# Performance work log

Hardware: AMD Instinct MI355X
Metric: run time of the kernel (lower is better)

## Reference

```python
import jax, jax.numpy as jnp
import numpy as np

N, E, D = 50000, 500000, 128


def layer_norm(x, w, b, eps=1e-5):
    mu = jnp.mean(x, axis=-1, keepdims=True)
    var = jnp.var(x, axis=-1, keepdims=True)
    return (x - mu) * jax.lax.rsqrt(var + eps) * w + b


def setup_inputs() -> dict:
    key = jax.random.key(0)
    ks = jax.random.split(key, 8)
    z = jax.random.normal(ks[0], (N, D), dtype=jnp.float32)
    pot_arcs = jax.random.randint(ks[1], (E, 2), 0, N, dtype=jnp.int64)
    s = 1.0 / np.sqrt(D)
    lin1_w = jax.random.uniform(ks[2], (D, D), jnp.float32, -s, s)
    lin1_b = jax.random.uniform(ks[3], (D,), jnp.float32, -s, s)
    lin2_w = jax.random.uniform(ks[4], (D, D), jnp.float32, -s, s)
    lin2_b = jax.random.uniform(ks[5], (D,), jnp.float32, -s, s)
    bil_w = jax.random.uniform(ks[6], (1, D, D), jnp.float32, -s, s)
    bil_b = jax.random.uniform(ks[7], (1,), jnp.float32, -s, s)
    norm_w = jnp.ones((D,), jnp.float32)
    norm_b = jnp.zeros((D,), jnp.float32)
    return {"z": z, "pot_arcs": pot_arcs, "lin1_w": lin1_w, "lin1_b": lin1_b,
            "lin2_w": lin2_w, "lin2_b": lin2_b, "bil_w": bil_w, "bil_b": bil_b,
            "norm_w": norm_w, "norm_b": norm_b}


def reference(z, pot_arcs, lin1_w, lin1_b, lin2_w, lin2_b, bil_w, bil_b, norm_w, norm_b):
    # shared LayerNorm on all nodes
    zn = layer_norm(z, norm_w, norm_b)                     # [N, D]
    x1 = zn[pot_arcs[:, 0]]                                # [E, D] gather heads
    x2 = zn[pot_arcs[:, 1]]                                # [E, D] gather tails
    # lin -> relu -> layernorm (dropout = identity at eval)
    h1 = layer_norm(jax.nn.relu(x1 @ lin1_w.T + lin1_b), norm_w, norm_b)
    h2 = layer_norm(jax.nn.relu(x2 @ lin2_w.T + lin2_b), norm_w, norm_b)
    # bilinear score: out_e = h1_e^T W h2_e + b, W = bil_w[0]
    score = jnp.einsum('ed,df,ef->e', h1, bil_w[0], h2) + bil_b[0]
    return score                                           # [E]
```

## Files before the change

kernel.cpp:

```cpp
#include <hip/hip_runtime.h>

#define D 128
#define TM 64

typedef __attribute__((ext_vector_type(8))) short short8v;
typedef __attribute__((ext_vector_type(4))) float float4v;

__device__ __forceinline__ unsigned short f2bf(float f) {
    unsigned int u = __float_as_uint(f);
    u += 0x7FFFu + ((u >> 16) & 1u);
    return (unsigned short)(u >> 16);
}
__device__ __forceinline__ float bflo(int u) {
    return __uint_as_float(((unsigned int)u) << 16);
}
__device__ __forceinline__ float bfhi(int u) {
    return __uint_as_float(((unsigned int)u) & 0xFFFF0000u);
}

__global__ __launch_bounds__(256) void wconv(
    const float* __restrict__ w1, const float* __restrict__ w2,
    const float* __restrict__ wb, unsigned short* __restrict__ dst)
{
    int tid = blockIdx.x * 256 + threadIdx.x;
    int w = tid >> 11;
    int r = tid & 2047;
    int l = r & 63;
    int tk = r >> 6;
    int t = tk >> 2, ks = tk & 3;
    int n = t * 16 + (l & 15);
    int k = ks * 32 + (l >> 4) * 8;
    const float* src = (w == 0) ? w1 : (w == 1) ? w2 : wb;
    const float* p = src + n * D + k;
    float4 a = *(const float4*)p;
    float4 b = *(const float4*)(p + 4);
    union { int4 i4; unsigned short u[8]; } pk;
    pk.u[0] = f2bf(a.x); pk.u[1] = f2bf(a.y); pk.u[2] = f2bf(a.z); pk.u[3] = f2bf(a.w);
    pk.u[4] = f2bf(b.x); pk.u[5] = f2bf(b.y); pk.u[6] = f2bf(b.z); pk.u[7] = f2bf(b.w);
    *(int4*)(dst + (size_t)tid * 8) = pk.i4;
}

__global__ __launch_bounds__(256) void node_kernel(
    const float* __restrict__ z,
    const unsigned short* __restrict__ wfrag,
    const float* __restrict__ lin1_b, const float* __restrict__ lin2_b,
    const float* __restrict__ norm_w, const float* __restrict__ norm_b,
    unsigned short* __restrict__ T1, unsigned short* __restrict__ T2,
    int N)
{
    __shared__ unsigned short sa[TM][136];
    __shared__ unsigned short sh[TM][136];

    const int tid  = threadIdx.x;
    const int lane = tid & 63;
    const int wave = tid >> 6;
    const int n0   = blockIdx.x * TM;
    const int cg   = lane & 15;
    const int q    = lane >> 4;

    {
        const int c = cg * 8;
        float4 nw0 = *(const float4*)(norm_w + c);
        float4 nw1 = *(const float4*)(norm_w + c + 4);
        float4 nb0 = *(const float4*)(norm_b + c);
        float4 nb1 = *(const float4*)(norm_b + c + 4);
        #pragma unroll
        for (int it = 0; it < 4; ++it) {
            int rr = wave * 16 + it * 4 + q;
            int n  = n0 + rr;
            int nc = (n < N) ? n : (N - 1);
            const float* zp = z + (size_t)nc * D + c;
            float4 v0 = *(const float4*)zp;
            float4 v1 = *(const float4*)(zp + 4);
            float s  = v0.x + v0.y + v0.z + v0.w + v1.x + v1.y + v1.z + v1.w;
            float qq = v0.x*v0.x + v0.y*v0.y + v0.z*v0.z + v0.w*v0.w
                     + v1.x*v1.x + v1.y*v1.y + v1.z*v1.z + v1.w*v1.w;
            #pragma unroll
            for (int m = 1; m <= 8; m <<= 1) {
                s  += __shfl_xor(s, m, 64);
                qq += __shfl_xor(qq, m, 64);
            }
            float mu  = s * (1.0f / D);
            float var = qq * (1.0f / D) - mu * mu;
            float rs  = rsqrtf(var + 1e-5f);
            union { int4 i4; unsigned short u[8]; } pk;
            pk.u[0] = f2bf((v0.x - mu) * rs * nw0.x + nb0.x);
            pk.u[1] = f2bf((v0.y - mu) * rs * nw0.y + nb0.y);
            pk.u[2] = f2bf((v0.z - mu) * rs * nw0.z + nb0.z);
            pk.u[3] = f2bf((v0.w - mu) * rs * nw0.w + nb0.w);
            pk.u[4] = f2bf((v1.x - mu) * rs * nw1.x + nb1.x);
            pk.u[5] = f2bf((v1.y - mu) * rs * nw1.y + nb1.y);
            pk.u[6] = f2bf((v1.z - mu) * rs * nw1.z + nb1.z);
            pk.u[7] = f2bf((v1.w - mu) * rs * nw1.w + nb1.w);
            *(int4*)&sa[rr][c] = pk.i4;
        }
    }
    __syncthreads();

    float4v acc[8];

    auto run_gemm = [&](const unsigned short (*A)[136], const unsigned short* wf) {
        #pragma unroll
        for (int t = 0; t < 8; ++t) acc[t] = (float4v)(0.0f);
        #pragma unroll
        for (int ks = 0; ks < 4; ++ks) {
            short8v a = *(const short8v*)&A[wave * 16 + cg][ks * 32 + q * 8];
            const short8v* wp = (const short8v*)wf + ks * 64 + lane;
            #pragma unroll
            for (int t = 0; t < 8; ++t) {
                short8v b = wp[t * 256];
                acc[t] = __builtin_amdgcn_mfma_f32_16x16x32_bf16(a, b, acc[t], 0, 0, 0);
            }
        }
    };

    auto epilogue_ln = [&](const float* lb) {
        float bia[8], nwv[8], nbv[8];
        #pragma unroll
        for (int t = 0; t < 8; ++t) {
            int col = t * 16 + cg;
            bia[t] = lb[col]; nwv[t] = norm_w[col]; nbv[t] = norm_b[col];
        }
        float s[4] = {0, 0, 0, 0}, qs[4] = {0, 0, 0, 0};
        #pragma unroll
        for (int t = 0; t < 8; ++t)
            #pragma unroll
            for (int i = 0; i < 4; ++i) {
                float v = fmaxf(acc[t][i] + bia[t], 0.0f);
                acc[t][i] = v;
                s[i] += v; qs[i] += v * v;
            }
        #pragma unroll
        for (int i = 0; i < 4; ++i) {
            #pragma unroll
            for (int m = 1; m <= 8; m <<= 1) {
                s[i]  += __shfl_xor(s[i], m, 64);
                qs[i] += __shfl_xor(qs[i], m, 64);
            }
        }
        #pragma unroll
        for (int i = 0; i < 4; ++i) {
            float mu  = s[i] * (1.0f / D);
            float var = qs[i] * (1.0f / D) - mu * mu;
            float rs  = rsqrtf(var + 1e-5f);
            s[i] = mu; qs[i] = rs;
        }
        #pragma unroll
        for (int t = 0; t < 8; ++t)
            #pragma unroll
            for (int i = 0; i < 4; ++i)
                sh[wave * 16 + q * 4 + i][t * 16 + cg] =
                    f2bf((acc[t][i] - s[i]) * qs[i] * nwv[t] + nbv[t]);
    };

    auto copyout = [&](const unsigned short (*S)[136], unsigned short* dst) {
        int r = tid >> 2;
        int n = n0 + r;
        if (n < N) {
            #pragma unroll
            for (int j = 0; j < 4; ++j) {
                int c = (tid & 3) * 8 + j * 32;
                int4 d = *(const int4*)&S[r][c];
                *(int4*)(dst + (size_t)n * D + c) = d;
            }
        }
    };

    run_gemm(sa, wfrag);
    epilogue_ln(lin1_b);
    __syncthreads();
    copyout(sh, T1);

    run_gemm(sa, wfrag + 16384);
    __syncthreads();
    epilogue_ln(lin2_b);
    __syncthreads();

    run_gemm(sh, wfrag + 32768);
    #pragma unroll
    for (int t = 0; t < 8; ++t)
        #pragma unroll
        for (int i = 0; i < 4; ++i)
            sa[wave * 16 + q * 4 + i][t * 16 + cg] = f2bf(acc[t][i]);
    __syncthreads();
    copyout(sa, T2);
}

__global__ __launch_bounds__(256) void arc_kernel(
    const int* __restrict__ arcs,
    const unsigned short* __restrict__ T1,
    const unsigned short* __restrict__ T2,
    const float* __restrict__ bil_b,
    float* __restrict__ out, int E)
{
    const int tid  = threadIdx.x;
    const int lane = tid & 63;
    long long gw = ((long long)blockIdx.x * 256 + tid) >> 6;
    long long e0 = gw * 8;
    int aidx = lane >> 3;
    int s    = lane & 7;

    long long ii = e0 * 2 + (lane & 15);
    long long iimax = (long long)E * 2 - 1;
    int iv = arcs[ii <= iimax ? ii : iimax];
    int a0 = __shfl(iv, aidx * 2, 64);
    int a1 = __shfl(iv, aidx * 2 + 1, 64);
    long long e = e0 + aidx;

    const int4* P = (const int4*)(T1 + (size_t)a0 * D);
    const int4* Q = (const int4*)(T2 + (size_t)a1 * D);
    int4 x0 = P[s];
    int4 x1 = P[s + 8];
    int4 y0 = Q[s];
    int4 y1 = Q[s + 8];

    float acc = 0.0f;
    acc += bflo(x0.x) * bflo(y0.x) + bfhi(x0.x) * bfhi(y0.x);
    acc += bflo(x0.y) * bflo(y0.y) + bfhi(x0.y) * bfhi(y0.y);
    acc += bflo(x0.z) * bflo(y0.z) + bfhi(x0.z) * bfhi(y0.z);
    acc += bflo(x0.w) * bflo(y0.w) + bfhi(x0.w) * bfhi(y0.w);
    acc += bflo(x1.x) * bflo(y1.x) + bfhi(x1.x) * bfhi(y1.x);
    acc += bflo(x1.y) * bflo(y1.y) + bfhi(x1.y) * bfhi(y1.y);
    acc += bflo(x1.z) * bflo(y1.z) + bfhi(x1.z) * bfhi(y1.z);
    acc += bflo(x1.w) * bflo(y1.w) + bfhi(x1.w) * bfhi(y1.w);

    #pragma unroll
    for (int m = 1; m <= 4; m <<= 1) acc += __shfl_xor(acc, m, 64);

    if (s == 0 && e < E) out[e] = acc + bil_b[0];
}

extern "C" void kernel_launch(void* const* d_in, const int* in_sizes, int n_in,
                              void* d_out, int out_size, void* d_ws, size_t ws_size,
                              hipStream_t stream) {
    const float* z      = (const float*)d_in[0];
    const int*   arcs   = (const int*)d_in[1];
    const float* lin1_w = (const float*)d_in[2];
    const float* lin1_b = (const float*)d_in[3];
    const float* lin2_w = (const float*)d_in[4];
    const float* lin2_b = (const float*)d_in[5];
    const float* bil_w  = (const float*)d_in[6];
    const float* bil_b  = (const float*)d_in[7];
    const float* norm_w = (const float*)d_in[8];
    const float* norm_b = (const float*)d_in[9];
    float* out = (float*)d_out;

    const int N = in_sizes[0] / D;
    const int E = in_sizes[1] / 2;

    unsigned short* wfrag = (unsigned short*)d_ws;
    unsigned short* T1 = wfrag + 3 * 16384;
    unsigned short* T2 = T1 + (size_t)N * D;

    wconv<<<24, 256, 0, stream>>>(lin1_w, lin2_w, bil_w, wfrag);

    node_kernel<<<(N + TM - 1) / TM, 256, 0, stream>>>(
        z, wfrag, lin1_b, lin2_b, norm_w, norm_b, T1, T2, N);

    long long waves = ((long long)E + 7) / 8;
    int blocks = (int)((waves + 3) / 4);
    arc_kernel<<<blocks, 256, 0, stream>>>(arcs, T1, T2, bil_b, out, E);
}
```

Before: 144.6 us.

## Fuse lin1/lin2 GEMMs, drop block barriers, and process 16 arcs per wave

The node kernel now runs the lin1 and lin2 MFMA GEMMs in one loop, sharing the A-fragment load, and keeps separate LDS buffers for the two LayerNorm outputs. Each wave touches only its own 16 rows, so all __syncthreads barriers are removed. The arc kernel changes to 4 lanes per arc and 16 arcs per wave, with more loads in flight per lane. The costs are higher register pressure from two accumulator sets and an extra LDS buffer, both of which may lower occupancy.

New measurement: 141.9 us. Within noise of the previous version (-1.9%).

```diff
diff --git a/kernel.cpp b/kernel.cpp
--- a/kernel.cpp
+++ b/kernel.cpp
@@ -48,15 +48,17 @@
     unsigned short* __restrict__ T1, unsigned short* __restrict__ T2,
     int N)
 {
-    __shared__ unsigned short sa[TM][136];
-    __shared__ unsigned short sh[TM][136];
-
-    const int tid  = threadIdx.x;
-    const int lane = tid & 63;
-    const int wave = tid >> 6;
-    const int n0   = blockIdx.x * TM;
-    const int cg   = lane & 15;
-    const int q    = lane >> 4;
+    __shared__ unsigned short sa [TM][136];
+    __shared__ unsigned short sh1[TM][136];
+    __shared__ unsigned short sh2[TM][136];
+
+    const int tid   = threadIdx.x;
+    const int lane  = tid & 63;
+    const int wave  = tid >> 6;
+    const int n0    = blockIdx.x * TM;
+    const int cg    = lane & 15;
+    const int q     = lane >> 4;
+    const int rbase = wave * 16;
 
     {
         const int c = cg * 8;
@@ -66,7 +68,7 @@
         float4 nb1 = *(const float4*)(norm_b + c + 4);
         #pragma unroll
         for (int it = 0; it < 4; ++it) {
-            int rr = wave * 16 + it * 4 + q;
+            int rr = rbase + it * 4 + q;
             int n  = n0 + rr;
             int nc = (n < N) ? n : (N - 1);
             const float* zp = z + (size_t)nc * D + c;
@@ -95,41 +97,33 @@
             *(int4*)&sa[rr][c] = pk.i4;
         }
     }
-    __syncthreads();
-
-    float4v acc[8];
-
-    auto run_gemm = [&](const unsigned short (*A)[136], const unsigned short* wf) {
-        #pragma unroll
-        for (int t = 0; t < 8; ++t) acc[t] = (float4v)(0.0f);
-        #pragma unroll
-        for (int ks = 0; ks < 4; ++ks) {
-            short8v a = *(const short8v*)&A[wave * 16 + cg][ks * 32 + q * 8];
-            const short8v* wp = (const short8v*)wf + ks * 64 + lane;
-            #pragma unroll
-            for (int t = 0; t < 8; ++t) {
-                short8v b = wp[t * 256];
-                acc[t] = __builtin_amdgcn_mfma_f32_16x16x32_bf16(a, b, acc[t], 0, 0, 0);
-            }
-        }
-    };
-
-    auto epilogue_ln = [&](const float* lb) {
-        float bia[8], nwv[8], nbv[8];
+
+    float4v acc1[8], acc2[8];
+    #pragma unroll
+    for (int t = 0; t < 8; ++t) { acc1[t] = (float4v)(0.0f); acc2[t] = (float4v)(0.0f); }
+    #pragma unroll
+    for (int ks = 0; ks < 4; ++ks) {
+        short8v a = *(const short8v*)&sa[rbase + cg][ks * 32 + q * 8];
+        const short8v* wp = (const short8v*)wfrag + ks * 64 + lane;
         #pragma unroll
         for (int t = 0; t < 8; ++t) {
-            int col = t * 16 + cg;
-            bia[t] = lb[col]; nwv[t] = norm_w[col]; nbv[t] = norm_b[col];
-        }
+            acc1[t] = __builtin_amdgcn_mfma_f32_16x16x32_bf16(a, wp[t * 256],        acc1[t], 0, 0, 0);
+            acc2[t] = __builtin_amdgcn_mfma_f32_16x16x32_bf16(a, wp[t * 256 + 2048], acc2[t], 0, 0, 0);
+        }
+    }
+
+    auto epilogue = [&](float4v* acc, const float* lb, unsigned short (*dst)[136]) {
         float s[4] = {0, 0, 0, 0}, qs[4] = {0, 0, 0, 0};
         #pragma unroll
-        for (int t = 0; t < 8; ++t)
+        for (int t = 0; t < 8; ++t) {
+            float b = lb[t * 16 + cg];
             #pragma unroll
             for (int i = 0; i < 4; ++i) {
-                float v = fmaxf(acc[t][i] + bia[t], 0.0f);
+                float v = fmaxf(acc[t][i] + b, 0.0f);
                 acc[t][i] = v;
                 s[i] += v; qs[i] += v * v;
             }
+        }
         #pragma unroll
         for (int i = 0; i < 4; ++i) {
             #pragma unroll
@@ -137,52 +131,51 @@
                 s[i]  += __shfl_xor(s[i], m, 64);
                 qs[i] += __shfl_xor(qs[i], m, 64);
             }
-        }
-        #pragma unroll
-        for (int i = 0; i < 4; ++i) {
             float mu  = s[i] * (1.0f / D);
             float var = qs[i] * (1.0f / D) - mu * mu;
-            float rs  = rsqrtf(var + 1e-5f);
-            s[i] = mu; qs[i] = rs;
-        }
-        #pragma unroll
-        for (int t = 0; t < 8; ++t)
+            s[i] = mu; qs[i] = rsqrtf(var + 1e-5f);
+        }
+        #pragma unroll
+        for (int t = 0; t < 8; ++t) {
+            int col = t * 16 + cg;
+            float nw = norm_w[col], nb = norm_b[col];
             #pragma unroll
             for (int i = 0; i < 4; ++i)
-                sh[wave * 16 + q * 4 + i][t * 16 + cg] =
-                    f2bf((acc[t][i] - s[i]) * qs[i] * nwv[t] + nbv[t]);
+                dst[rbase + q * 4 + i][col] = f2bf((acc[t][i] - s[i]) * qs[i] * nw + nb);
+        }
     };
 
     auto copyout = [&](const unsigned short (*S)[136], unsigned short* dst) {
-        int r = tid >> 2;
+        int r = rbase + (lane >> 2);
         int n = n0 + r;
         if (n < N) {
             #pragma unroll
             for (int j = 0; j < 4; ++j) {
-                int c = (tid & 3) * 8 + j * 32;
-                int4 d = *(const int4*)&S[r][c];
-                *(int4*)(dst + (size_t)n * D + c) = d;
+                int c = (lane & 3) * 8 + j * 32;
+                *(int4*)(dst + (size_t)n * D + c) = *(const int4*)&S[r][c];
             }
         }
     };
 
-    run_gemm(sa, wfrag);
-    epilogue_ln(lin1_b);
-    __syncthreads();
-    copyout(sh, T1);
-
-    run_gemm(sa, wfrag + 16384);
-    __syncthreads();
-    epilogue_ln(lin2_b);
-    __syncthreads();
-
-    run_gemm(sh, wfrag + 32768);
+    epilogue(acc1, lin1_b, sh1);
+    epilogue(acc2, lin2_b, sh2);
+    copyout(sh1, T1);
+
+    #pragma unroll
+    for (int t = 0; t < 8; ++t) acc1[t] = (float4v)(0.0f);
+    #pragma unroll
+    for (int ks = 0; ks < 4; ++ks) {
+        short8v a = *(const short8v*)&sh2[rbase + cg][ks * 32 + q * 8];
+        const short8v* wp = (const short8v*)wfrag + 4096 + ks * 64 + lane;
+        #pragma unroll
+        for (int t = 0; t < 8; ++t)
+            acc1[t] = __builtin_amdgcn_mfma_f32_16x16x32_bf16(a, wp[t * 256], acc1[t], 0, 0, 0);
+    }
     #pragma unroll
     for (int t = 0; t < 8; ++t)
         #pragma unroll
         for (int i = 0; i < 4; ++i)
-            sa[wave * 16 + q * 4 + i][t * 16 + cg] = f2bf(acc[t][i]);
-    __syncthreads();
+            sa[rbase + q * 4 + i][t * 16 + cg] = f2bf(acc1[t][i]);
     copyout(sa, T2);
 }
 
@@ -196,11 +189,11 @@
     const int tid  = threadIdx.x;
     const int lane = tid & 63;
     long long gw = ((long long)blockIdx.x * 256 + tid) >> 6;
-    long long e0 = gw * 8;
-    int aidx = lane >> 3;
-    int s    = lane & 7;
-
-    long long ii = e0 * 2 + (lane & 15);
+    long long e0 = gw * 16;
+    int aidx = lane >> 2;
+    int s    = lane & 3;
+
+    long long ii = e0 * 2 + (lane & 31);
     long long iimax = (long long)E * 2 - 1;
     int iv = arcs[ii <= iimax ? ii : iimax];
     int a0 = __shfl(iv, aidx * 2, 64);
@@ -210,22 +203,34 @@
     const int4* P = (const int4*)(T1 + (size_t)a0 * D);
     const int4* Q = (const int4*)(T2 + (size_t)a1 * D);
     int4 x0 = P[s];
-    int4 x1 = P[s + 8];
+    int4 x1 = P[s + 4];
+    int4 x2 = P[s + 8];
+    int4 x3 = P[s + 12];
     int4 y0 = Q[s];
-    int4 y1 = Q[s + 8];
+    int4 y1 = Q[s + 4];
+    int4 y2 = Q[s + 8];
+    int4 y3 = Q[s + 12];
 
     float acc = 0.0f;
-    acc += bflo(x0.x) * bflo(y0.x) + bfhi(x0.x) * bfhi(y0.x);
-    acc += bflo(x0.y) * bflo(y0.y) + bfhi(x0.y) * bfhi(y0.y);
-    acc += bflo(x0.z) * bflo(y0.z) + bfhi(x0.z) * bfhi(y0.z);
-    acc += bflo(x0.w) * bflo(y0.w) + bfhi(x0.w) * bfhi(y0.w);
-    acc += bflo(x1.x) * bflo(y1.x) + bfhi(x1.x) * bfhi(y1.x);
-    acc += bflo(x1.y) * bflo(y1.y) + bfhi(x1.y) * bfhi(y1.y);
-    acc += bflo(x1.z) * bflo(y1.z) + bfhi(x1.z) * bfhi(y1.z);
-    acc += bflo(x1.w) * bflo(y1.w) + bfhi(x1.w) * bfhi(y1.w);
-
-    #pragma unroll
-    for (int m = 1; m <= 4; m <<= 1) acc += __shfl_xor(acc, m, 64);
+    acc += bflo(x0.x)*bflo(y0.x) + bfhi(x0.x)*bfhi(y0.x);
+    acc += bflo(x0.y)*bflo(y0.y) + bfhi(x0.y)*bfhi(y0.y);
+    acc += bflo(x0.z)*bflo(y0.z) + bfhi(x0.z)*bfhi(y0.z);
+    acc += bflo(x0.w)*bflo(y0.w) + bfhi(x0.w)*bfhi(y0.w);
+    acc += bflo(x1.x)*bflo(y1.x) + bfhi(x1.x)*bfhi(y1.x);
+    acc += bflo(x1.y)*bflo(y1.y) + bfhi(x1.y)*bfhi(y1.y);
+    acc += bflo(x1.z)*bflo(y1.z) + bfhi(x1.z)*bfhi(y1.z);
+    acc += bflo(x1.w)*bflo(y1.w) + bfhi(x1.w)*bfhi(y1.w);
+    acc += bflo(x2.x)*bflo(y2.x) + bfhi(x2.x)*bfhi(y2.x);
+    acc += bflo(x2.y)*bflo(y2.y) + bfhi(x2.y)*bfhi(y2.y);
+    acc += bflo(x2.z)*bflo(y2.z) + bfhi(x2.z)*bfhi(y2.z);
+    acc += bflo(x2.w)*bflo(y2.w) + bfhi(x2.w)*bfhi(y2.w);
+    acc += bflo(x3.x)*bflo(y3.x) + bfhi(x3.x)*bfhi(y3.x);
+    acc += bflo(x3.y)*bflo(y3.y) + bfhi(x3.y)*bfhi(y3.y);
+    acc += bflo(x3.z)*bflo(y3.z) + bfhi(x3.z)*bfhi(y3.z);
+    acc += bflo(x3.w)*bflo(y3.w) + bfhi(x3.w)*bfhi(y3.w);
+
+    acc += __shfl_xor(acc, 1, 64);
+    acc += __shfl_xor(acc, 2, 64);
 
     if (s == 0 && e < E) out[e] = acc + bil_b[0];
 }
@@ -257,7 +262,7 @@
     node_kernel<<<(N + TM - 1) / TM, 256, 0, stream>>>(
         z, wfrag, lin1_b, lin2_b, norm_w, norm_b, T1, T2, N);
 
-    long long waves = ((long long)E + 7) / 8;
+    long long waves = ((long long)E + 15) / 16;
     int blocks = (int)((waves + 3) / 4);
     arc_kernel<<<blocks, 256, 0, stream>>>(arcs, T1, T2, bil_b, out, E);
 }
```
